# Kernel optimization log

Hardware: AMD Instinct MI355X
Metric: run time of the kernel (lower is better)

Reference implementation:

```python
import jax, jax.numpy as jnp
import numpy as np

MINC, MAXC, RATIO = 1, 16, 0.25


def _upsample2x(x):
    # bilinear, align_corners=False, (h,w) -> (2h,2w)
    B, C, h, w = x.shape
    def idx(n_in, n_out):
        src = (jnp.arange(n_out) + 0.5) * (n_in / n_out) - 0.5
        i0f = jnp.floor(src)
        t = (src - i0f).astype(jnp.float32)
        i0 = jnp.clip(i0f, 0, n_in - 1).astype(jnp.int32)
        i1 = jnp.clip(i0f + 1, 0, n_in - 1).astype(jnp.int32)
        return i0, i1, t
    i0, i1, t = idx(h, 2 * h)
    x = x[:, :, i0, :] * (1 - t)[None, None, :, None] + x[:, :, i1, :] * t[None, None, :, None]
    j0, j1, s = idx(w, 2 * w)
    x = x[:, :, :, j0] * (1 - s)[None, None, None, :] + x[:, :, :, j1] * s[None, None, None, :]
    return x


def _connection_counts(x):
    # DFDetector: down(0.5 bilinear, no antialias) == 2x2 avg-pool for even H,W
    B, C, H, W = x.shape
    xd = x.reshape(B, C, H // 2, 2, W // 2, 2).mean(axis=(3, 5))
    xu = _upsample2x(xd)
    df = jnp.abs(x - xu).sum(axis=1)  # [B,H,W]
    dmin = df.reshape(B, -1).min(axis=1)[:, None, None]
    dmax = df.reshape(B, -1).max(axis=1)[:, None, None]
    dn = (df - dmin) / (dmax - dmin + 1e-8)
    return (MINC + jnp.round(dn * (MAXC - MINC))).astype(jnp.int32)  # [B,H,W]


def setup_inputs() -> dict:
    key = jax.random.key(0)
    k0, k1, k2 = jax.random.split(key, 3)
    C = 64
    return {
        "x": jax.random.normal(k0, (2, C, 64, 64), jnp.float32),
        "ln_gamma": jnp.ones((C,), jnp.float32),
        "ln_beta": jnp.zeros((C,), jnp.float32),
        "w1": jax.random.normal(k1, (2 * C, C), jnp.float32) * 0.05,
        "b1": jnp.zeros((2 * C,), jnp.float32),
        "w2": jax.random.normal(k2, (C, 2 * C), jnp.float32) * 0.05,
        "b2": jnp.zeros((C,), jnp.float32),
    }


def reference(x, ln_gamma, ln_beta, w1, b1, w2, b2):
    B, C, H, W = x.shape
    k = _connection_counts(x).reshape(B, H * W)  # [B,HW] in [1,16]

    win = max(3, int(min(H, W) * RATIO))
    win += (win % 2 == 0)  # 17 for 64x64
    half = win // 2
    offs = np.arange(-half, half + 1)
    dy = np.repeat(offs, win); dx = np.tile(offs, win)             # [K2]
    py = np.repeat(np.arange(H), W); px = np.tile(np.arange(W), H)  # [HW]
    ny = py[:, None] + dy[None, :]; nx = px[:, None] + dx[None, :]
    valid = jnp.asarray((ny >= 0) & (ny < H) & (nx >= 0) & (nx < W))          # [HW,K2]
    idx = jnp.asarray(np.clip(ny, 0, H - 1) * W + np.clip(nx, 0, W - 1))      # [HW,K2]

    x_flat = x.transpose(0, 2, 3, 1).reshape(B, H * W, C)
    xn = x_flat / jnp.maximum(jnp.linalg.norm(x_flat, axis=-1, keepdims=True), 1e-12)

    nbr = xn[:, idx]                                   # [B,HW,K2,C]
    sim = jnp.einsum('bpc,bpkc->bpk', xn, nbr)         # cosine similarity
    sim = jnp.where(valid[None], sim, -1e30)           # mask out-of-bounds

    top_sim, top_i = jax.lax.top_k(sim, MAXC)          # [B,HW,16]
    mask = (jnp.arange(MAXC)[None, None, :] < k[:, :, None]).astype(x.dtype)
    wts = jnp.exp(top_sim) * mask
    wts = wts / wts.sum(-1, keepdims=True)

    gidx = jnp.take_along_axis(jnp.broadcast_to(idx[None], (B,) + idx.shape), top_i, axis=2)
    feats = jax.vmap(lambda xf, gi: xf[gi])(x_flat, gidx)  # [B,HW,16,C]
    agg = jnp.einsum('bpk,bpkc->bpc', wts, feats)
    out = agg.reshape(B, H, W, C).transpose(0, 3, 1, 2)

    # per-pixel channel LayerNorm (intent of nn.LayerNorm([C,1,1]))
    mu = x.mean(axis=1, keepdims=True)
    var = ((x - mu) ** 2).mean(axis=1, keepdims=True)
    xln = (x - mu) / jnp.sqrt(var + 1e-5) * ln_gamma[None, :, None, None] + ln_beta[None, :, None, None]

    enh = out + xln
    h1 = jax.nn.relu(jnp.einsum('bchw,dc->bdhw', enh, w1) + b1[None, :, None, None])
    ffn = jnp.einsum('bdhw,cd->bchw', h1, w2) + b2[None, :, None, None]
    return enh + ffn
```

## Files before the change

kernel.cpp:

```cpp
#include <hip/hip_runtime.h>
#include <math.h>

#define BB  2
#define CC  64
#define HH  64
#define WW  64
#define PP  4096
#define CHW 262144
#define KMAX 16
#define NSL 432
#define SSTR 436

#define OFF_XT   0
#define OFF_XNH  524288
#define OFF_XNL  786432
#define OFF_DF   1048576
#define OFF_PMN  1056768
#define OFF_PMX  1057024

typedef __bf16 bf16x8 __attribute__((ext_vector_type(8)));
typedef __bf16 bf16x4 __attribute__((ext_vector_type(4)));
typedef float  f32x4  __attribute__((ext_vector_type(4)));

#define DPP_STEP(v, ctrl, OP) { int _s = __builtin_amdgcn_update_dpp( \
    __float_as_int(v), __float_as_int(v), ctrl, 0xf, 0xf, false); \
    v = OP(v, __int_as_float(_s)); }
__device__ __forceinline__ float addf_(float a, float b) { return a + b; }
__device__ __forceinline__ float wave_max_b(float v) {
    DPP_STEP(v, 0x111, fmaxf) DPP_STEP(v, 0x112, fmaxf) DPP_STEP(v, 0x114, fmaxf)
    DPP_STEP(v, 0x118, fmaxf) DPP_STEP(v, 0x142, fmaxf) DPP_STEP(v, 0x143, fmaxf)
    return __int_as_float(__builtin_amdgcn_readlane(__float_as_int(v), 63));
}
__device__ __forceinline__ float wave_min_b(float v) {
    DPP_STEP(v, 0x111, fminf) DPP_STEP(v, 0x112, fminf) DPP_STEP(v, 0x114, fminf)
    DPP_STEP(v, 0x118, fminf) DPP_STEP(v, 0x142, fminf) DPP_STEP(v, 0x143, fminf)
    return __int_as_float(__builtin_amdgcn_readlane(__float_as_int(v), 63));
}
__device__ __forceinline__ float wave_sum_b(float v) {
    DPP_STEP(v, 0x111, addf_) DPP_STEP(v, 0x112, addf_) DPP_STEP(v, 0x114, addf_)
    DPP_STEP(v, 0x118, addf_) DPP_STEP(v, 0x142, addf_) DPP_STEP(v, 0x143, addf_)
    return __int_as_float(__builtin_amdgcn_readlane(__float_as_int(v), 63));
}

__global__ __launch_bounds__(256) void k_prep(const float* __restrict__ x,
        float* __restrict__ xt,
        unsigned short* __restrict__ xnh, unsigned short* __restrict__ xnl,
        float* __restrict__ df, float* __restrict__ pmn, float* __restrict__ pmx) {
    __shared__ float T[64*33];
    __shared__ float xds[2304];
    __shared__ float pdf[8*33], pss[8*33];
    __shared__ float sinv[32];
    int t = threadIdx.x;
    int bp0 = blockIdx.x * 32;
    int b = bp0 >> 12, p0 = bp0 & 4095;
    int y = p0 >> 6, x0 = p0 & 63;
    const float* xb = x + b*CHW + p0;
    #pragma unroll
    for (int i = 0; i < 8; ++i) {
        int idx = t + i*256;
        int c = idx >> 5, pxl = idx & 31;
        T[c*33 + pxl] = xb[c*PP + pxl];
    }
    int m = y >> 1;
    int R0, R1; float ty;
    if ((y & 1) == 0) { R0 = m > 0 ? m-1 : 0; R1 = m; ty = 0.75f; }
    else              { R0 = m; R1 = m < 31 ? m+1 : 31; ty = 0.25f; }
    int h0 = x0 >> 1;
    #pragma unroll
    for (int i = 0; i < 9; ++i) {
        int id = t + i*256;
        int c = id / 36, rem = id - c*36;
        int rr = (rem >= 18) ? 1 : 0, cc = rem - rr*18;
        int row = rr ? R1 : R0;
        int col = h0 - 1 + cc; col = col < 0 ? 0 : (col > 31 ? 31 : col);
        const float* xp = x + b*CHW + c*PP + row*2*WW + col*2;
        float2 a0 = *(const float2*)xp;
        float2 a1 = *(const float2*)(xp + WW);
        xds[id] = (a0.x + a0.y + a1.x + a1.y) * 0.25f;
    }
    __syncthreads();
    int px = t & 31, sl = t >> 5;
    int xxp = x0 + px;
    int n2 = xxp >> 1, jx0, jx1; float tx;
    if ((xxp & 1) == 0) { jx0 = n2 > 0 ? n2-1 : 0; jx1 = n2; tx = 0.75f; }
    else                { jx0 = n2; jx1 = n2 < 31 ? n2+1 : 31; tx = 0.25f; }
    int cc0 = jx0 - h0 + 1, cc1 = jx1 - h0 + 1;
    float dfa = 0.f, ss = 0.f;
    #pragma unroll
    for (int ci = 0; ci < 8; ++ci) {
        int c = sl*8 + ci;
        const float* xc = &xds[c*36];
        float a00 = xc[cc0],      a10 = xc[18 + cc0];
        float a01 = xc[cc1],      a11 = xc[18 + cc1];
        float r0 = a00*(1.f-ty) + a10*ty;
        float r1 = a01*(1.f-ty) + a11*ty;
        float xu = r0*(1.f-tx) + r1*tx;
        float v = T[c*33 + px];
        dfa += fabsf(v - xu);
        ss  += v*v;
    }
    pdf[sl*33 + px] = dfa; pss[sl*33 + px] = ss;
    __syncthreads();
    if (t < 32) {
        float d = 0.f, s = 0.f;
        #pragma unroll
        for (int q = 0; q < 8; ++q) { d += pdf[q*33 + t]; s += pss[q*33 + t]; }
        df[bp0 + t] = d;
        sinv[t] = 1.f / fmaxf(sqrtf(s), 1e-12f);
        float mn = d, mx = d;
        #pragma unroll
        for (int off = 1; off < 32; off <<= 1) {
            mn = fminf(mn, __shfl_xor(mn, off));
            mx = fmaxf(mx, __shfl_xor(mx, off));
        }
        if (t == 0) { pmn[blockIdx.x] = mn; pmx[blockIdx.x] = mx; }
    }
    __syncthreads();
    int px2 = t >> 3, cg = t & 7;
    float inv = sinv[px2];
    int bp = bp0 + px2;
    float4 f0, f1; bf16x8 hh, ll;
    #pragma unroll
    for (int k = 0; k < 8; ++k) {
        float v = T[(cg*8 + k)*33 + px2];
        if (k < 4) ((float*)&f0)[k] = v; else ((float*)&f1)[k-4] = v;
        float xnv = v * inv;
        __bf16 hb = (__bf16)xnv;
        float lo = xnv - (float)hb;
        hh[k] = hb; ll[k] = (__bf16)lo;
    }
    *(float4*)&xt[bp*64 + cg*8]     = f0;
    *(float4*)&xt[bp*64 + cg*8 + 4] = f1;
    *(bf16x8*)&xnh[bp*64 + cg*8] = hh;
    *(bf16x8*)&xnl[bp*64 + cg*8] = ll;
}

__global__ __launch_bounds__(1024) void k_fuse(
        const unsigned short* __restrict__ xnh,
        const unsigned short* __restrict__ xnl,
        const float* __restrict__ xt, const float* __restrict__ df,
        const float* __restrict__ pmn, const float* __restrict__ pmx,
        const float* __restrict__ gamma, const float* __restrict__ beta,
        const float* __restrict__ w1, const float* __restrict__ b1,
        const float* __restrict__ w2, const float* __restrict__ b2,
        float* __restrict__ out) {
    __shared__ float  simsL[16*SSTR];
    __shared__ __bf16 w1bf[128*72];
    __shared__ __bf16 w2bf[64*136];
    __shared__ __bf16 enh16[16*72];
    __shared__ __bf16 h1bf[16*136];
    __shared__ float  enhT32[16*68];
    __shared__ float  smm[2];
    int t = threadIdx.x;
    int bid = blockIdx.x;
    int b = bid >> 8, tyi = (bid >> 3) & 31, txi = bid & 7;
    int y0 = tyi*2, x0 = txi*8;
    int pbase = (b << 12) + y0*64 + x0;
    int pix0 = pbase & 4095;
    int wv = t >> 6, lane = t & 63;
    int lr = lane & 15, lq = lane >> 4;
    #pragma unroll
    for (int j = 0; j < 2; ++j) {
        int i4 = t + j*1024;
        float4 v = *(const float4*)(w1 + i4*4);
        int dd = i4 >> 4, c0 = (i4 & 15)*4;
        bf16x4 h; h[0]=(__bf16)v.x; h[1]=(__bf16)v.y; h[2]=(__bf16)v.z; h[3]=(__bf16)v.w;
        *(bf16x4*)&w1bf[dd*72 + c0] = h;
    }
    #pragma unroll
    for (int j = 0; j < 2; ++j) {
        int i4 = t + j*1024;
        float4 v = *(const float4*)(w2 + i4*4);
        int cc2 = i4 >> 5, d0 = (i4 & 31)*4;
        bf16x4 h; h[0]=(__bf16)v.x; h[1]=(__bf16)v.y; h[2]=(__bf16)v.z; h[3]=(__bf16)v.w;
        *(bf16x4*)&w2bf[cc2*136 + d0] = h;
    }
    if (t < 64) {
        float v = fminf(pmn[b*128 + t], pmn[b*128 + 64 + t]);
        v = wave_min_b(v);
        if (t == 0) smm[0] = v;
    } else if (t < 128) {
        int u = t & 63;
        float v = fmaxf(pmx[b*128 + u], pmx[b*128 + 64 + u]);
        v = wave_max_b(v);
        if (u == 0) smm[1] = v;
    }
    {
        int bpA = pbase + ((lr >> 3) << 6) + (lr & 7);
        const unsigned short* ah = xnh + bpA*64 + lq*8;
        const unsigned short* al = xnl + bpA*64 + lq*8;
        bf16x8 ah0 = *(const bf16x8*)ah, ah1 = *(const bf16x8*)(ah + 32);
        bf16x8 al0 = *(const bf16x8*)al, al1 = *(const bf16x8*)(al + 32);
        for (int nt = wv; nt < 27; nt += 16) {
            int S = nt*16 + lr;
            int rr = S / 24, cc = S - rr*24;
            int ny = y0 + rr - 8, nx = x0 + cc - 8;
            bool vimg = ((unsigned)ny < 64u) && ((unsigned)nx < 64u);
            int bq = vimg ? ((b << 12) + ny*64 + nx) : pbase;
            const unsigned short* bh = xnh + bq*64 + lq*8;
            const unsigned short* bl = xnl + bq*64 + lq*8;
            bf16x8 bh0 = *(const bf16x8*)bh, bh1 = *(const bf16x8*)(bh + 32);
            bf16x8 bl0 = *(const bf16x8*)bl, bl1 = *(const bf16x8*)(bl + 32);
            f32x4 acc = (f32x4){0.f,0.f,0.f,0.f};
            acc = __builtin_amdgcn_mfma_f32_16x16x32_bf16(ah0, bh0, acc, 0, 0, 0);
            acc = __builtin_amdgcn_mfma_f32_16x16x32_bf16(ah0, bl0, acc, 0, 0, 0);
            acc = __builtin_amdgcn_mfma_f32_16x16x32_bf16(al0, bh0, acc, 0, 0, 0);
            acc = __builtin_amdgcn_mfma_f32_16x16x32_bf16(ah1, bh1, acc, 0, 0, 0);
            acc = __builtin_amdgcn_mfma_f32_16x16x32_bf16(ah1, bl1, acc, 0, 0, 0);
            acc = __builtin_amdgcn_mfma_f32_16x16x32_bf16(al1, bh1, acc, 0, 0, 0);
            #pragma unroll
            for (int r = 0; r < 4; ++r) {
                int pxo = lq*4 + r;
                simsL[pxo*SSTR + S] = vimg ? acc[r] : -1e30f;
            }
        }
    }
    __syncthreads();
    {
        int i_loc = wv >> 3, j_loc = wv & 7;
        int bp = pbase + i_loc*64 + j_loc;
        const float* srow = &simsL[wv*SSTR];
        float tv[7];
        #pragma unroll
        for (int j = 0; j < 7; ++j) {
            int s = lane + (j << 6);
            bool in = (j < 6) || (lane < 48);
            int rr = s / 24, cc = s - rr*24;
            int sy = rr - i_loc, sx = cc - j_loc;
            bool ok = in && ((unsigned)sy <= 16u) && ((unsigned)sx <= 16u);
            tv[j] = ok ? srow[s] : -1e30f;
        }
        float lbv = tv[0]; int lbj = 0;
        #pragma unroll
        for (int j = 1; j < 7; ++j) if (tv[j] > lbv) { lbv = tv[j]; lbj = j; }
        float dmin = smm[0], dmax = smm[1];
        float dn = (df[bp] - dmin) / (dmax - dmin + 1e-8f);
        int kk = 1 + (int)rintf(dn * 15.f);
        float xv = xt[bp*64 + lane];
        float su = wave_sum_b(xv);
        float sq = wave_sum_b(xv*xv);
        float mu = su * (1.f/64.f);
        float var = sq * (1.f/64.f) - mu*mu;
        float bvsave = 0.f; int ssave = 200;
        for (int rnd = 0; rnd < kk; ++rnd) {
            float bv = wave_max_b(lbv);
            unsigned long long msk = __ballot(lbv == bv);
            int src = __ffsll(msk) - 1;
            int js = __builtin_amdgcn_readlane(lbj, src);
            int s = src + (js << 6);
            if (lane == rnd) { bvsave = bv; ssave = s; }
            if (lane == src) {
                #pragma unroll
                for (int j = 0; j < 7; ++j) if (j == lbj) tv[j] = -3e30f;
            }
            lbv = tv[0]; lbj = 0;
            #pragma unroll
            for (int j = 1; j < 7; ++j) if (tv[j] > lbv) { lbv = tv[j]; lbj = j; }
        }
        float ee = (lane < kk) ? __expf(bvsave) : 0.f;
        float S = wave_sum_b(ee);
        int rr2 = ssave / 24, cc2 = ssave - rr2*24;
        int qq = pbase + (rr2 - 8)*64 + (cc2 - 8);
        float acc = 0.f;
        #pragma unroll
        for (int g = 0; g < 4; ++g) {
            if (g*4 >= kk) break;
            float e0 = __shfl(ee, g*4+0), e1 = __shfl(ee, g*4+1);
            float e2 = __shfl(ee, g*4+2), e3 = __shfl(ee, g*4+3);
            int   q0 = __shfl(qq, g*4+0), q1 = __shfl(qq, g*4+1);
            int   q2 = __shfl(qq, g*4+2), q3 = __shfl(qq, g*4+3);
            float v0 = xt[q0*64 + lane], v1 = xt[q1*64 + lane];
            float v2 = xt[q2*64 + lane], v3 = xt[q3*64 + lane];
            acc += e0*v0; acc += e1*v1; acc += e2*v2; acc += e3*v3;
        }
        float xln = (xv - mu) / sqrtf(var + 1e-5f) * gamma[lane] + beta[lane];
        float val = acc / S + xln;
        enhT32[wv*68 + lane] = val;
        enh16[wv*72 + lane] = (__bf16)val;
    }
    __syncthreads();
    if (wv < 8) {
        int d0 = wv*16;
        f32x4 acc1 = (f32x4){0.f,0.f,0.f,0.f};
        #pragma unroll
        for (int kh = 0; kh < 2; ++kh) {
            int kb = kh*32 + lq*8;
            bf16x8 a  = *(bf16x8*)&enh16[lr*72 + kb];
            bf16x8 bb = *(bf16x8*)&w1bf[(d0 + lr)*72 + kb];
            acc1 = __builtin_amdgcn_mfma_f32_16x16x32_bf16(a, bb, acc1, 0, 0, 0);
        }
        int dd = d0 + lr;
        float bias = b1[dd];
        #pragma unroll
        for (int r = 0; r < 4; ++r) {
            int pxr = lq*4 + r;
            h1bf[pxr*136 + dd] = (__bf16)fmaxf(acc1[r] + bias, 0.f);
        }
    }
    __syncthreads();
    if (wv < 4) {
        int c0 = wv*16;
        f32x4 acc2 = (f32x4){0.f,0.f,0.f,0.f};
        #pragma unroll
        for (int kh = 0; kh < 4; ++kh) {
            int kb = kh*32 + lq*8;
            bf16x8 a  = *(bf16x8*)&h1bf[lr*136 + kb];
            bf16x8 bb = *(bf16x8*)&w2bf[(c0 + lr)*136 + kb];
            acc2 = __builtin_amdgcn_mfma_f32_16x16x32_bf16(a, bb, acc2, 0, 0, 0);
        }
        int c = c0 + lr;
        float bias = b2[c];
        #pragma unroll
        for (int r = 0; r < 4; ++r) {
            int pxr = lq*4 + r;
            int pix = pix0 + ((pxr >> 3) << 6) + (pxr & 7);
            out[b*CHW + c*PP + pix] = acc2[r] + bias + enhT32[pxr*68 + c];
        }
    }
}

extern "C" void kernel_launch(void* const* d_in, const int* in_sizes, int n_in,
                              void* d_out, int out_size, void* d_ws, size_t ws_size,
                              hipStream_t stream) {
    const float* x     = (const float*)d_in[0];
    const float* gamma = (const float*)d_in[1];
    const float* beta  = (const float*)d_in[2];
    const float* w1    = (const float*)d_in[3];
    const float* b1    = (const float*)d_in[4];
    const float* w2    = (const float*)d_in[5];
    const float* b2    = (const float*)d_in[6];
    float* ws  = (float*)d_ws;
    float* xt  = ws + OFF_XT;
    float* df  = ws + OFF_DF;
    float* pmn = ws + OFF_PMN;
    float* pmx = ws + OFF_PMX;
    unsigned short* xnh = (unsigned short*)(ws + OFF_XNH);
    unsigned short* xnl = (unsigned short*)(ws + OFF_XNL);
    float* out = (float*)d_out;

    k_prep<<<256, 256, 0, stream>>>(x, xt, xnh, xnl, df, pmn, pmx);
    k_fuse<<<512, 1024, 0, stream>>>(xnh, xnl, xt, df, pmn, pmx, gamma, beta,
                                     w1, b1, w2, b2, out);
}
```

Before: 33.01 us.

## Double pixel tile per block and alias weight buffers over similarity scratch

Each block now handles a 4x8 pixel tile (32 pixels) instead of 2x8, so the grid halves to 256 blocks. Neighbour B-fragments are loaded once and feed two sets of MFMAs, which amortises the neighbour loads and the per-block weight conversion. Shared memory is unioned: the bf16 weight and FFN buffers reuse the similarity scratch space after top-k, so the weight staging moves after the selection phase. In exchange each wave does two top-k selections serially, and fewer blocks than CUs may leave parallelism unused.

```diff
diff --git a/kernel.cpp b/kernel.cpp
--- a/kernel.cpp
+++ b/kernel.cpp
@@ -8,8 +8,8 @@
 #define PP  4096
 #define CHW 262144
 #define KMAX 16
-#define NSL 432
-#define SSTR 436
+#define NSL 480
+#define SSTR 484
 
 #define OFF_XT   0
 #define OFF_XNH  524288
@@ -17,6 +17,12 @@
 #define OFF_DF   1048576
 #define OFF_PMN  1056768
 #define OFF_PMX  1057024
+
+#define TS_W1  0
+#define TS_W2  18432
+#define TS_H1  35840
+#define TS_E16 44544
+#define TS_E32 49152
 
 typedef __bf16 bf16x8 __attribute__((ext_vector_type(8)));
 typedef __bf16 bf16x4 __attribute__((ext_vector_type(4)));
@@ -144,37 +150,23 @@
         const float* __restrict__ w1, const float* __restrict__ b1,
         const float* __restrict__ w2, const float* __restrict__ b2,
         float* __restrict__ out) {
-    __shared__ float  simsL[16*SSTR];
-    __shared__ __bf16 w1bf[128*72];
-    __shared__ __bf16 w2bf[64*136];
-    __shared__ __bf16 enh16[16*72];
-    __shared__ __bf16 h1bf[16*136];
-    __shared__ float  enhT32[16*68];
-    __shared__ float  smm[2];
+    __shared__ __align__(16) char U[32*SSTR*4];
+    float* simsL = (float*)U;
+    __bf16* w1bf  = (__bf16*)(U + TS_W1);
+    __bf16* w2bf  = (__bf16*)(U + TS_W2);
+    __bf16* h1bf  = (__bf16*)(U + TS_H1);
+    __bf16* enh16 = (__bf16*)(U + TS_E16);
+    float*  enhT32= (float*)(U + TS_E32);
+    __shared__ float smm[2];
     int t = threadIdx.x;
     int bid = blockIdx.x;
-    int b = bid >> 8, tyi = (bid >> 3) & 31, txi = bid & 7;
-    int y0 = tyi*2, x0 = txi*8;
+    int b = bid >> 7, tid = bid & 127;
+    int tyi = tid >> 3, txi = tid & 7;
+    int y0 = tyi*4, x0 = txi*8;
     int pbase = (b << 12) + y0*64 + x0;
     int pix0 = pbase & 4095;
     int wv = t >> 6, lane = t & 63;
     int lr = lane & 15, lq = lane >> 4;
-    #pragma unroll
-    for (int j = 0; j < 2; ++j) {
-        int i4 = t + j*1024;
-        float4 v = *(const float4*)(w1 + i4*4);
-        int dd = i4 >> 4, c0 = (i4 & 15)*4;
-        bf16x4 h; h[0]=(__bf16)v.x; h[1]=(__bf16)v.y; h[2]=(__bf16)v.z; h[3]=(__bf16)v.w;
-        *(bf16x4*)&w1bf[dd*72 + c0] = h;
-    }
-    #pragma unroll
-    for (int j = 0; j < 2; ++j) {
-        int i4 = t + j*1024;
-        float4 v = *(const float4*)(w2 + i4*4);
-        int cc2 = i4 >> 5, d0 = (i4 & 31)*4;
-        bf16x4 h; h[0]=(__bf16)v.x; h[1]=(__bf16)v.y; h[2]=(__bf16)v.z; h[3]=(__bf16)v.w;
-        *(bf16x4*)&w2bf[cc2*136 + d0] = h;
-    }
     if (t < 64) {
         float v = fminf(pmn[b*128 + t], pmn[b*128 + 64 + t]);
         v = wave_min_b(v);
@@ -186,12 +178,18 @@
         if (u == 0) smm[1] = v;
     }
     {
-        int bpA = pbase + ((lr >> 3) << 6) + (lr & 7);
-        const unsigned short* ah = xnh + bpA*64 + lq*8;
-        const unsigned short* al = xnl + bpA*64 + lq*8;
-        bf16x8 ah0 = *(const bf16x8*)ah, ah1 = *(const bf16x8*)(ah + 32);
-        bf16x8 al0 = *(const bf16x8*)al, al1 = *(const bf16x8*)(al + 32);
-        for (int nt = wv; nt < 27; nt += 16) {
+        int pxa0 = lr, pxa1 = 16 + lr;
+        int bpA0 = pbase + ((pxa0 >> 3) << 6) + (pxa0 & 7);
+        int bpA1 = pbase + ((pxa1 >> 3) << 6) + (pxa1 & 7);
+        const unsigned short* a0p = xnh + bpA0*64 + lq*8;
+        const unsigned short* a0l = xnl + bpA0*64 + lq*8;
+        const unsigned short* a1p = xnh + bpA1*64 + lq*8;
+        const unsigned short* a1l = xnl + bpA1*64 + lq*8;
+        bf16x8 A0h0 = *(const bf16x8*)a0p, A0h1 = *(const bf16x8*)(a0p + 32);
+        bf16x8 A0l0 = *(const bf16x8*)a0l, A0l1 = *(const bf16x8*)(a0l + 32);
+        bf16x8 A1h0 = *(const bf16x8*)a1p, A1h1 = *(const bf16x8*)(a1p + 32);
+        bf16x8 A1l0 = *(const bf16x8*)a1l, A1l1 = *(const bf16x8*)(a1l + 32);
+        for (int nt = wv; nt < 30; nt += 16) {
             int S = nt*16 + lr;
             int rr = S / 24, cc = S - rr*24;
             int ny = y0 + rr - 8, nx = x0 + cc - 8;
@@ -201,30 +199,41 @@
             const unsigned short* bl = xnl + bq*64 + lq*8;
             bf16x8 bh0 = *(const bf16x8*)bh, bh1 = *(const bf16x8*)(bh + 32);
             bf16x8 bl0 = *(const bf16x8*)bl, bl1 = *(const bf16x8*)(bl + 32);
-            f32x4 acc = (f32x4){0.f,0.f,0.f,0.f};
-            acc = __builtin_amdgcn_mfma_f32_16x16x32_bf16(ah0, bh0, acc, 0, 0, 0);
-            acc = __builtin_amdgcn_mfma_f32_16x16x32_bf16(ah0, bl0, acc, 0, 0, 0);
-            acc = __builtin_amdgcn_mfma_f32_16x16x32_bf16(al0, bh0, acc, 0, 0, 0);
-            acc = __builtin_amdgcn_mfma_f32_16x16x32_bf16(ah1, bh1, acc, 0, 0, 0);
-            acc = __builtin_amdgcn_mfma_f32_16x16x32_bf16(ah1, bl1, acc, 0, 0, 0);
-            acc = __builtin_amdgcn_mfma_f32_16x16x32_bf16(al1, bh1, acc, 0, 0, 0);
+            f32x4 ac0 = (f32x4){0.f,0.f,0.f,0.f};
+            f32x4 ac1 = (f32x4){0.f,0.f,0.f,0.f};
+            ac0 = __builtin_amdgcn_mfma_f32_16x16x32_bf16(A0h0, bh0, ac0, 0, 0, 0);
+            ac0 = __builtin_amdgcn_mfma_f32_16x16x32_bf16(A0h0, bl0, ac0, 0, 0, 0);
+            ac0 = __builtin_amdgcn_mfma_f32_16x16x32_bf16(A0l0, bh0, ac0, 0, 0, 0);
+            ac0 = __builtin_amdgcn_mfma_f32_16x16x32_bf16(A0h1, bh1, ac0, 0, 0, 0);
+            ac0 = __builtin_amdgcn_mfma_f32_16x16x32_bf16(A0h1, bl1, ac0, 0, 0, 0);
+            ac0 = __builtin_amdgcn_mfma_f32_16x16x32_bf16(A0l1, bh1, ac0, 0, 0, 0);
+            ac1 = __builtin_amdgcn_mfma_f32_16x16x32_bf16(A1h0, bh0, ac1, 0, 0, 0);
+            ac1 = __builtin_amdgcn_mfma_f32_16x16x32_bf16(A1h0, bl0, ac1, 0, 0, 0);
+            ac1 = __builtin_amdgcn_mfma_f32_16x16x32_bf16(A1l0, bh0, ac1, 0, 0, 0);
+            ac1 = __builtin_amdgcn_mfma_f32_16x16x32_bf16(A1h1, bh1, ac1, 0, 0, 0);
+            ac1 = __builtin_amdgcn_mfma_f32_16x16x32_bf16(A1h1, bl1, ac1, 0, 0, 0);
+            ac1 = __builtin_amdgcn_mfma_f32_16x16x32_bf16(A1l1, bh1, ac1, 0, 0, 0);
             #pragma unroll
             for (int r = 0; r < 4; ++r) {
-                int pxo = lq*4 + r;
-                simsL[pxo*SSTR + S] = vimg ? acc[r] : -1e30f;
+                int p0r = lq*4 + r;
+                simsL[p0r*SSTR + S]        = vimg ? ac0[r] : -1e30f;
+                simsL[(16 + p0r)*SSTR + S] = vimg ? ac1[r] : -1e30f;
             }
         }
     }
     __syncthreads();
-    {
-        int i_loc = wv >> 3, j_loc = wv & 7;
+    float val[2];
+    #pragma unroll
+    for (int ii = 0; ii < 2; ++ii) {
+        int px = wv*2 + ii;
+        int i_loc = px >> 3, j_loc = px & 7;
         int bp = pbase + i_loc*64 + j_loc;
-        const float* srow = &simsL[wv*SSTR];
-        float tv[7];
-        #pragma unroll
-        for (int j = 0; j < 7; ++j) {
+        const float* srow = &simsL[px*SSTR];
+        float tv[8];
+        #pragma unroll
+        for (int j = 0; j < 8; ++j) {
             int s = lane + (j << 6);
-            bool in = (j < 6) || (lane < 48);
+            bool in = (j < 7) || (lane < 32);
             int rr = s / 24, cc = s - rr*24;
             int sy = rr - i_loc, sx = cc - j_loc;
             bool ok = in && ((unsigned)sy <= 16u) && ((unsigned)sx <= 16u);
@@ -232,7 +241,7 @@
         }
         float lbv = tv[0]; int lbj = 0;
         #pragma unroll
-        for (int j = 1; j < 7; ++j) if (tv[j] > lbv) { lbv = tv[j]; lbj = j; }
+        for (int j = 1; j < 8; ++j) if (tv[j] > lbv) { lbv = tv[j]; lbj = j; }
         float dmin = smm[0], dmax = smm[1];
         float dn = (df[bp] - dmin) / (dmax - dmin + 1e-8f);
         int kk = 1 + (int)rintf(dn * 15.f);
@@ -251,11 +260,11 @@
             if (lane == rnd) { bvsave = bv; ssave = s; }
             if (lane == src) {
                 #pragma unroll
-                for (int j = 0; j < 7; ++j) if (j == lbj) tv[j] = -3e30f;
+                for (int j = 0; j < 8; ++j) if (j == lbj) tv[j] = -3e30f;
             }
             lbv = tv[0]; lbj = 0;
             #pragma unroll
-            for (int j = 1; j < 7; ++j) if (tv[j] > lbv) { lbv = tv[j]; lbj = j; }
+            for (int j = 1; j < 8; ++j) if (tv[j] > lbv) { lbv = tv[j]; lbj = j; }
         }
         float ee = (lane < kk) ? __expf(bvsave) : 0.f;
         float S = wave_sum_b(ee);
@@ -274,18 +283,39 @@
             acc += e0*v0; acc += e1*v1; acc += e2*v2; acc += e3*v3;
         }
         float xln = (xv - mu) / sqrtf(var + 1e-5f) * gamma[lane] + beta[lane];
-        float val = acc / S + xln;
-        enhT32[wv*68 + lane] = val;
-        enh16[wv*72 + lane] = (__bf16)val;
-    }
-    __syncthreads();
-    if (wv < 8) {
-        int d0 = wv*16;
+        val[ii] = acc / S + xln;
+    }
+    __syncthreads();
+    #pragma unroll
+    for (int j = 0; j < 2; ++j) {
+        int i4 = t + j*1024;
+        float4 v = *(const float4*)(w1 + i4*4);
+        int dd = i4 >> 4, c0 = (i4 & 15)*4;
+        bf16x4 h; h[0]=(__bf16)v.x; h[1]=(__bf16)v.y; h[2]=(__bf16)v.z; h[3]=(__bf16)v.w;
+        *(bf16x4*)&w1bf[dd*72 + c0] = h;
+    }
+    #pragma unroll
+    for (int j = 0; j < 2; ++j) {
+        int i4 = t + j*1024;
+        float4 v = *(const float4*)(w2 + i4*4);
+        int cc2 = i4 >> 5, d0 = (i4 & 31)*4;
+        bf16x4 h; h[0]=(__bf16)v.x; h[1]=(__bf16)v.y; h[2]=(__bf16)v.z; h[3]=(__bf16)v.w;
+        *(bf16x4*)&w2bf[cc2*136 + d0] = h;
+    }
+    #pragma unroll
+    for (int ii = 0; ii < 2; ++ii) {
+        int px = wv*2 + ii;
+        enhT32[px*68 + lane] = val[ii];
+        enh16[px*72 + lane] = (__bf16)val[ii];
+    }
+    __syncthreads();
+    {
+        int mblk = wv & 1, d0 = (wv >> 1)*16;
         f32x4 acc1 = (f32x4){0.f,0.f,0.f,0.f};
         #pragma unroll
         for (int kh = 0; kh < 2; ++kh) {
             int kb = kh*32 + lq*8;
-            bf16x8 a  = *(bf16x8*)&enh16[lr*72 + kb];
+            bf16x8 a  = *(bf16x8*)&enh16[(mblk*16 + lr)*72 + kb];
             bf16x8 bb = *(bf16x8*)&w1bf[(d0 + lr)*72 + kb];
             acc1 = __builtin_amdgcn_mfma_f32_16x16x32_bf16(a, bb, acc1, 0, 0, 0);
         }
@@ -293,18 +323,18 @@
         float bias = b1[dd];
         #pragma unroll
         for (int r = 0; r < 4; ++r) {
-            int pxr = lq*4 + r;
+            int pxr = mblk*16 + lq*4 + r;
             h1bf[pxr*136 + dd] = (__bf16)fmaxf(acc1[r] + bias, 0.f);
         }
     }
     __syncthreads();
-    if (wv < 4) {
-        int c0 = wv*16;
+    if (wv < 8) {
+        int mblk = wv & 1, c0 = (wv >> 1)*16;
         f32x4 acc2 = (f32x4){0.f,0.f,0.f,0.f};
         #pragma unroll
         for (int kh = 0; kh < 4; ++kh) {
             int kb = kh*32 + lq*8;
-            bf16x8 a  = *(bf16x8*)&h1bf[lr*136 + kb];
+            bf16x8 a  = *(bf16x8*)&h1bf[(mblk*16 + lr)*136 + kb];
             bf16x8 bb = *(bf16x8*)&w2bf[(c0 + lr)*136 + kb];
             acc2 = __builtin_amdgcn_mfma_f32_16x16x32_bf16(a, bb, acc2, 0, 0, 0);
         }
@@ -312,7 +342,7 @@
         float bias = b2[c];
         #pragma unroll
         for (int r = 0; r < 4; ++r) {
-            int pxr = lq*4 + r;
+            int pxr = mblk*16 + lq*4 + r;
             int pix = pix0 + ((pxr >> 3) << 6) + (pxr & 7);
             out[b*CHW + c*PP + pix] = acc2[r] + bias + enhT32[pxr*68 + c];
         }
@@ -339,6 +369,6 @@
     float* out = (float*)d_out;
 
     k_prep<<<256, 256, 0, stream>>>(x, xt, xnh, xnl, df, pmn, pmx);
-    k_fuse<<<512, 1024, 0, stream>>>(xnh, xnl, xt, df, pmn, pmx, gamma, beta,
+    k_fuse<<<256, 1024, 0, stream>>>(xnh, xnl, xt, df, pmn, pmx, gamma, beta,
                                      w1, b1, w2, b2, out);
 }
```

Result: slower. 36.60 us (+10.9%).
